# Kernel tuning notes

Hardware: AMD Instinct MI355X
Metric: run time of the kernel (lower is better)

## Reference

```python
import jax, jax.numpy as jnp
import numpy as np

N, F, E, T = 50000, 128, 800000, 8


def setup_inputs() -> dict:
    key = jax.random.key(0)
    ks = jax.random.split(key, 10)
    s = 1.0 / np.sqrt(F)
    return {
        "x": jax.random.normal(ks[0], (N, F), jnp.float32),
        "edge_index": jax.random.randint(ks[1], (2, E), 0, N, jnp.int64),
        "edge_weight": jax.random.uniform(ks[2], (E,), jnp.float32),
        "W0": jax.random.normal(ks[3], (F, F), jnp.float32) * s,
        "Wih": jax.random.normal(ks[4], (3 * F, F), jnp.float32) * s,
        "Whh": jax.random.normal(ks[5], (3 * F, F), jnp.float32) * s,
        "bih": jax.random.normal(ks[6], (3 * F,), jnp.float32) * s,
        "bhh": jax.random.normal(ks[7], (3 * F,), jnp.float32) * s,
        "Wlin": jax.random.normal(ks[8], (T, F), jnp.float32) * s,
        "blin": jax.random.normal(ks[9], (T,), jnp.float32) * s,
    }


def _evolve_weight(W0, Wih, Whh, bih, bhh):
    # One GRU step with input = hidden = W0 (rows of weight matrix as batch).
    gi = W0 @ Wih.T + bih  # [F, 3F]
    gh = W0 @ Whh.T + bhh
    ir, iz, inn = jnp.split(gi, 3, axis=1)
    hr, hz, hn = jnp.split(gh, 3, axis=1)
    r = jax.nn.sigmoid(ir + hr)
    z = jax.nn.sigmoid(iz + hz)
    n = jnp.tanh(inn + r * hn)
    return (1.0 - z) * n + z * W0  # [F, F]


def reference(x, edge_index, edge_weight, W0, Wih, Whh, bih, bhh, Wlin, blin):
    n_nodes = x.shape[0]
    W = _evolve_weight(W0, Wih, Whh, bih, bhh)
    # gcn_norm with added self-loops (fill value 1.0), symmetric normalization
    loop = jnp.arange(n_nodes, dtype=edge_index.dtype)
    row = jnp.concatenate([edge_index[0], loop])
    col = jnp.concatenate([edge_index[1], loop])
    ew = jnp.concatenate([edge_weight, jnp.ones((n_nodes,), edge_weight.dtype)])
    deg = jax.ops.segment_sum(ew, col, num_segments=n_nodes)
    dinv = jnp.where(deg > 0, jax.lax.rsqrt(jnp.where(deg > 0, deg, 1.0)), 0.0)
    norm = dinv[row] * ew * dinv[col]  # [E+N]
    xw = x @ W  # [N, F]
    h = jax.ops.segment_sum(norm[:, None] * xw[row], col, num_segments=n_nodes)
    h = jax.nn.relu(h)
    return h @ Wlin.T + blin  # [N, n_target]
```

## Files before the change

### kernel.cpp

```cpp
#include <hip/hip_runtime.h>
#include <math.h>

#define F 128
#define FIX_SCALE 16777216.0f
#define FIX_INV   (1.0f / 16777216.0f)
#define CNT_SHIFT 40
#define DEG_MASK  ((1ULL << 40) - 1)

using bf16x8 = __attribute__((ext_vector_type(8))) short;
using f32x4  = __attribute__((ext_vector_type(4))) float;

__device__ inline int read_idx(const int* ei, long long elem, int i64) {
    return i64 ? (int)((const long long*)ei)[elem] : ei[elem];
}
__device__ inline unsigned int f2bf_rn(float f) {
    unsigned int b = __float_as_uint(f);
    return (b + 0x7FFFu + ((b >> 16) & 1u)) >> 16;
}
__device__ inline float bflo(unsigned int u) { return __uint_as_float(u << 16); }
__device__ inline float bfhi(unsigned int u) { return __uint_as_float(u & 0xFFFF0000u); }

__device__ inline void acc8(float* acc, float wt, uint4 v) {
    acc[0] += wt * bflo(v.x); acc[1] += wt * bfhi(v.x);
    acc[2] += wt * bflo(v.y); acc[3] += wt * bfhi(v.y);
    acc[4] += wt * bflo(v.z); acc[5] += wt * bfhi(v.z);
    acc[6] += wt * bflo(v.w); acc[7] += wt * bfhi(v.w);
}

__global__ void k_init(unsigned long long* packed, int* flag, const int* ei, int N) {
    int i = blockIdx.x * blockDim.x + threadIdx.x;
    if (i < N) packed[i] = 0ULL;
    if (i == 0) {
        int i64 = 1;
        for (int j = 0; j < 32; ++j) if (ei[2 * j + 1] != 0) { i64 = 0; break; }
        *flag = i64;
    }
}

__global__ __launch_bounds__(256) void k_count_evolve(
        const int* __restrict__ ei, const float* __restrict__ ew,
        unsigned long long* __restrict__ packed, int* __restrict__ pos,
        const int* __restrict__ flag, int E, int cntBlocks,
        const float* __restrict__ W0, const float* __restrict__ Wih,
        const float* __restrict__ Whh, const float* __restrict__ bih,
        const float* __restrict__ bhh,
        unsigned short* __restrict__ Wth, unsigned short* __restrict__ Wtl) {
    __shared__ __align__(16) float w0row[F];
    if ((int)blockIdx.x < cntBlocks) {
        int e = blockIdx.x * 256 + threadIdx.x;
        if (e >= E) return;
        int i64 = *flag;
        int c = read_idx(ei, (long long)E + e, i64);
        unsigned long long u = (1ULL << CNT_SHIFT) |
                               (unsigned long long)(ew[e] * FIX_SCALE + 0.5f);
        unsigned long long old = atomicAdd(&packed[c], u);
        pos[e] = (int)(old >> CNT_SHIFT);
        return;
    }
    int i = blockIdx.x - cntBlocks;
    int j = threadIdx.x;
    if (j < F) w0row[j] = W0[i * F + j];
    __syncthreads();
    if (j >= F) return;
    float air = 0, aiz = 0, ain = 0, ahr = 0, ahz = 0, ahn = 0;
    const float* ir_p = Wih + (size_t)j * F;
    const float* iz_p = Wih + (size_t)(j + F) * F;
    const float* in_p = Wih + (size_t)(j + 2 * F) * F;
    const float* hr_p = Whh + (size_t)j * F;
    const float* hz_p = Whh + (size_t)(j + F) * F;
    const float* hn_p = Whh + (size_t)(j + 2 * F) * F;
    for (int k = 0; k < F; k += 4) {
        float4 w0 = *(const float4*)&w0row[k];
        float4 a;
        a = *(const float4*)&ir_p[k]; air += w0.x*a.x + w0.y*a.y + w0.z*a.z + w0.w*a.w;
        a = *(const float4*)&iz_p[k]; aiz += w0.x*a.x + w0.y*a.y + w0.z*a.z + w0.w*a.w;
        a = *(const float4*)&in_p[k]; ain += w0.x*a.x + w0.y*a.y + w0.z*a.z + w0.w*a.w;
        a = *(const float4*)&hr_p[k]; ahr += w0.x*a.x + w0.y*a.y + w0.z*a.z + w0.w*a.w;
        a = *(const float4*)&hz_p[k]; ahz += w0.x*a.x + w0.y*a.y + w0.z*a.z + w0.w*a.w;
        a = *(const float4*)&hn_p[k]; ahn += w0.x*a.x + w0.y*a.y + w0.z*a.z + w0.w*a.w;
    }
    air += bih[j];         ahr += bhh[j];
    aiz += bih[j + F];     ahz += bhh[j + F];
    ain += bih[j + 2*F];   ahn += bhh[j + 2*F];
    float r = 1.0f / (1.0f + expf(-(air + ahr)));
    float z = 1.0f / (1.0f + expf(-(aiz + ahz)));
    float n = tanhf(ain + r * ahn);
    float w = (1.0f - z) * n + z * w0row[j];
    unsigned int hb = f2bf_rn(w);
    float whi = __uint_as_float(hb << 16);
    unsigned int lb = f2bf_rn(w - whi);
    Wth[j * F + i] = (unsigned short)hb;
    Wtl[j * F + i] = (unsigned short)lb;
}

__global__ void k_bsum(const unsigned long long* __restrict__ packed,
                       int* __restrict__ bsum, int N) {
    __shared__ int s[4];
    int i = blockIdx.x * 256 + threadIdx.x;
    int v = (i < N) ? (int)(packed[i] >> CNT_SHIFT) : 0;
    #pragma unroll
    for (int o = 1; o < 64; o <<= 1) v += __shfl_xor(v, o, 64);
    if ((threadIdx.x & 63) == 0) s[threadIdx.x >> 6] = v;
    __syncthreads();
    if (threadIdx.x == 0) bsum[blockIdx.x] = s[0] + s[1] + s[2] + s[3];
}

__global__ void k_bscan(int* bsum, int nb) {
    __shared__ int sdata[1024];
    int tid = threadIdx.x;
    int run = 0;
    for (int base = 0; base < nb; base += 1024) {
        int i = base + tid;
        int v = (i < nb) ? bsum[i] : 0;
        sdata[tid] = v;
        __syncthreads();
        #pragma unroll
        for (int s = 1; s < 1024; s <<= 1) {
            int add = (tid >= s) ? sdata[tid - s] : 0;
            __syncthreads();
            sdata[tid] += add;
            __syncthreads();
        }
        if (i < nb) bsum[i] = run + sdata[tid] - v;
        run += sdata[1023];
        __syncthreads();
    }
}

__global__ void k_offs(const unsigned long long* __restrict__ packed,
                       const int* __restrict__ bsum,
                       int* __restrict__ off, float* __restrict__ dinv, int N, int E) {
    __shared__ int sdata[256];
    int t = threadIdx.x;
    int i = blockIdx.x * 256 + t;
    unsigned long long p = (i < N) ? packed[i] : 0ULL;
    int v = (int)(p >> CNT_SHIFT);
    sdata[t] = v;
    __syncthreads();
    #pragma unroll
    for (int s = 1; s < 256; s <<= 1) {
        int add = (t >= s) ? sdata[t - s] : 0;
        __syncthreads();
        sdata[t] += add;
        __syncthreads();
    }
    if (i < N) {
        off[i] = bsum[blockIdx.x] + sdata[t] - v;
        float deg = 1.0f + (float)(p & DEG_MASK) * FIX_INV;
        dinv[i] = rsqrtf(deg);
        if (i == N - 1) off[N] = E;
    }
}

__global__ __launch_bounds__(256) void k_place_cast(
        const int* __restrict__ ei, const float* __restrict__ ew,
        const int* __restrict__ off, const int* __restrict__ pos,
        int2* __restrict__ ep, const int* __restrict__ flag, int E, int placeBlocks,
        const float2* __restrict__ x2, const float* __restrict__ dinv,
        unsigned int* __restrict__ xs, int M) {
    if ((int)blockIdx.x < placeBlocks) {
        int e = blockIdx.x * 256 + threadIdx.x;
        if (e >= E) return;
        int i64 = *flag;
        int r = read_idx(ei, e, i64);
        int c = read_idx(ei, (long long)E + e, i64);
        ep[off[c] + pos[e]] = make_int2(r, __float_as_int(ew[e]));
    } else {
        int id = ((int)blockIdx.x - placeBlocks) * 256 + threadIdx.x;
        if (id >= M) return;
        float di = dinv[id >> 6];
        float2 v = x2[id];
        xs[id] = f2bf_rn(di * v.x) | (f2bf_rn(di * v.y) << 16);
    }
}

__global__ __launch_bounds__(256) void k_agg2(const uint4* __restrict__ xs4,
                                              const int* __restrict__ off,
                                              const int2* __restrict__ ep,
                                              const float* __restrict__ dinv,
                                              uint4* __restrict__ hagg4, int N) {
    int wave = threadIdx.x >> 6, lane = threadIdx.x & 63;
    int c = blockIdx.x * 4 + wave;
    if (c >= N) return;
    int g = lane >> 4, sl = lane & 15;
    int start = off[c], end = off[c + 1];
    float di = dinv[c];
    float a0[8] = {0,0,0,0,0,0,0,0}, a1[8] = {0,0,0,0,0,0,0,0};
    if (g == 0) {
        uint4 v = xs4[(size_t)c * 16 + sl];
        a0[0] = bflo(v.x); a0[1] = bfhi(v.x);
        a0[2] = bflo(v.y); a0[3] = bfhi(v.y);
        a0[4] = bflo(v.z); a0[5] = bfhi(v.z);
        a0[6] = bflo(v.w); a0[7] = bfhi(v.w);
    }
    int last = end - 1;
    for (int k = start; k < end; k += 16) {
        int iA = k + g, iB = k + g + 4, iC = k + g + 8, iD = k + g + 12;
        int2 eA = ep[min(iA, last)];
        int2 eB = ep[min(iB, last)];
        int2 eC = ep[min(iC, last)];
        int2 eD = ep[min(iD, last)];
        uint4 vA = xs4[(size_t)eA.x * 16 + sl];
        uint4 vB = xs4[(size_t)eB.x * 16 + sl];
        uint4 vC = xs4[(size_t)eC.x * 16 + sl];
        uint4 vD = xs4[(size_t)eD.x * 16 + sl];
        float wA = (iA <= last) ? __int_as_float(eA.y) : 0.f;
        float wB = (iB <= last) ? __int_as_float(eB.y) : 0.f;
        float wC = (iC <= last) ? __int_as_float(eC.y) : 0.f;
        float wD = (iD <= last) ? __int_as_float(eD.y) : 0.f;
        acc8(a0, wA, vA);
        acc8(a1, wB, vB);
        acc8(a0, wC, vC);
        acc8(a1, wD, vD);
    }
    #pragma unroll
    for (int f = 0; f < 8; ++f) {
        float v = a0[f] + a1[f];
        v += __shfl_xor(v, 16, 64);
        v += __shfl_xor(v, 32, 64);
        a0[f] = v;
    }
    if (lane < 16) {
        uint4 o;
        o.x = f2bf_rn(di * a0[0]) | (f2bf_rn(di * a0[1]) << 16);
        o.y = f2bf_rn(di * a0[2]) | (f2bf_rn(di * a0[3]) << 16);
        o.z = f2bf_rn(di * a0[4]) | (f2bf_rn(di * a0[5]) << 16);
        o.w = f2bf_rn(di * a0[6]) | (f2bf_rn(di * a0[7]) << 16);
        hagg4[(size_t)c * 16 + lane] = o;
    }
}

__global__ __launch_bounds__(256) void k_gemm(const uint4* __restrict__ hagg4,
                                              const unsigned short* __restrict__ Wth,
                                              const unsigned short* __restrict__ Wtl,
                                              const float* __restrict__ Wlin,
                                              const float* __restrict__ blin,
                                              float* __restrict__ out, int N) {
    __shared__ __align__(16) unsigned int At[64 * 68];
    __shared__ __align__(16) float WlinL[8 * F];
    int t = threadIdx.x;
    int row0 = blockIdx.x * 64;
    #pragma unroll
    for (int it = 0; it < 4; ++it) {
        int idx = it * 256 + t;
        int rr = idx >> 4, c4 = idx & 15;
        uint4 v = make_uint4(0u, 0u, 0u, 0u);
        if (row0 + rr < N) v = hagg4[(size_t)(row0 + rr) * 16 + c4];
        *(uint4*)&At[rr * 68 + c4 * 4] = v;
    }
    *(float4*)&WlinL[t * 4] = *(const float4*)&Wlin[t * 4];
    __syncthreads();

    int wave = t >> 6, lane = t & 63;
    int sl = lane & 15, q = lane >> 4;
    const unsigned short* Ash = (const unsigned short*)At;
    int mrow = wave * 16 + sl;

    f32x4 acc[8];
    #pragma unroll
    for (int nt = 0; nt < 8; ++nt) acc[nt] = (f32x4){0.f, 0.f, 0.f, 0.f};
    #pragma unroll
    for (int ko = 0; ko < 4; ++ko) {
        bf16x8 a = *(const bf16x8*)&Ash[mrow * 136 + ko * 32 + q * 8];
        #pragma unroll
        for (int nt = 0; nt < 8; ++nt) {
            int boff = (nt * 16 + sl) * F + ko * 32 + q * 8;
            bf16x8 bh = *(const bf16x8*)&Wth[boff];
            bf16x8 bl = *(const bf16x8*)&Wtl[boff];
            acc[nt] = __builtin_amdgcn_mfma_f32_16x16x32_bf16(a, bh, acc[nt], 0, 0, 0);
            acc[nt] = __builtin_amdgcn_mfma_f32_16x16x32_bf16(a, bl, acc[nt], 0, 0, 0);
        }
    }
    #pragma unroll
    for (int nt = 0; nt < 8; ++nt)
        #pragma unroll
        for (int r = 0; r < 4; ++r) acc[nt][r] = fmaxf(acc[nt][r], 0.f);

    float p[8][4];
    #pragma unroll
    for (int tt = 0; tt < 8; ++tt) {
        float wl[8];
        #pragma unroll
        for (int nt = 0; nt < 8; ++nt) wl[nt] = WlinL[tt * F + nt * 16 + sl];
        #pragma unroll
        for (int r = 0; r < 4; ++r) {
            float s = 0.f;
            #pragma unroll
            for (int nt = 0; nt < 8; ++nt) s += acc[nt][r] * wl[nt];
            p[tt][r] = s;
        }
    }
    #pragma unroll
    for (int tt = 0; tt < 8; ++tt)
        #pragma unroll
        for (int r = 0; r < 4; ++r) {
            float v = p[tt][r];
            v += __shfl_xor(v, 1, 64); v += __shfl_xor(v, 2, 64);
            v += __shfl_xor(v, 4, 64); v += __shfl_xor(v, 8, 64);
            p[tt][r] = v;
        }
    if (sl == 0) {
        #pragma unroll
        for (int r = 0; r < 4; ++r) {
            int row = row0 + wave * 16 + q * 4 + r;
            if (row < N) {
                #pragma unroll
                for (int tt = 0; tt < 8; ++tt)
                    out[(size_t)row * 8 + tt] = p[tt][r] + blin[tt];
            }
        }
    }
}

extern "C" void kernel_launch(void* const* d_in, const int* in_sizes, int n_in,
                              void* d_out, int out_size, void* d_ws, size_t ws_size,
                              hipStream_t stream) {
    const float* x    = (const float*)d_in[0];
    const int*   ei   = (const int*)d_in[1];
    const float* ew   = (const float*)d_in[2];
    const float* W0   = (const float*)d_in[3];
    const float* Wih  = (const float*)d_in[4];
    const float* Whh  = (const float*)d_in[5];
    const float* bih  = (const float*)d_in[6];
    const float* bhh  = (const float*)d_in[7];
    const float* Wlin = (const float*)d_in[8];
    const float* blin = (const float*)d_in[9];
    int N = in_sizes[0] / F;
    int E = in_sizes[1] / 2;
    float* outp = (float*)d_out;

    int nblk = (N + 255) / 256;
    int cntBlocks = (E + 255) / 256;
    int M = N * 64;

    char* wsb = (char*)d_ws;
    size_t cur = 0;
    auto alloc = [&](size_t sz) -> void* {
        void* p = wsb + cur;
        cur = (cur + sz + 255) & ~(size_t)255;
        return p;
    };
    unsigned long long* packed = (unsigned long long*)alloc((size_t)N * 8);
    float* dinv = (float*)alloc((size_t)N * 4);
    int*   off  = (int*)  alloc((size_t)(N + 1) * 4);
    int*   bsum = (int*)  alloc((size_t)nblk * 4);
    int*   flag = (int*)  alloc(256);
    int*   pos  = (int*)  alloc((size_t)E * 4);
    int2*  ep   = (int2*) alloc((size_t)E * 8);
    unsigned short* Wth = (unsigned short*)alloc((size_t)F * F * 2);
    unsigned short* Wtl = (unsigned short*)alloc((size_t)F * F * 2);
    unsigned int* xs    = (unsigned int*)alloc((size_t)N * 64 * 4);
    unsigned int* hagg  = (unsigned int*)alloc((size_t)N * 64 * 4);
    (void)ws_size; (void)n_in; (void)out_size;

    hipLaunchKernelGGL(k_init, dim3(nblk), dim3(256), 0, stream, packed, flag, ei, N);
    hipLaunchKernelGGL(k_count_evolve, dim3(cntBlocks + F), dim3(256), 0, stream,
                       ei, ew, packed, pos, flag, E, cntBlocks,
                       W0, Wih, Whh, bih, bhh, Wth, Wtl);
    hipLaunchKernelGGL(k_bsum,  dim3(nblk), dim3(256),  0, stream, packed, bsum, N);
    hipLaunchKernelGGL(k_bscan, dim3(1),    dim3(1024), 0, stream, bsum, nblk);
    hipLaunchKernelGGL(k_offs,  dim3(nblk), dim3(256),  0, stream, packed, bsum, off, dinv, N, E);
    hipLaunchKernelGGL(k_place_cast, dim3(cntBlocks + (M + 255) / 256), dim3(256), 0, stream,
                       ei, ew, off, pos, ep, flag, E, cntBlocks,
                       (const float2*)x, dinv, xs, M);
    hipLaunchKernelGGL(k_agg2, dim3((N + 3) / 4), dim3(256), 0, stream,
                       (const uint4*)xs, off, ep, dinv, (uint4*)hagg, N);
    hipLaunchKernelGGL(k_gemm, dim3((N + 63) / 64), dim3(256), 0, stream,
                       (const uint4*)hagg, Wth, Wtl, Wlin, blin, outp, N);
}
```

Baseline: 249.9 us.

## Privatize degree atomics across eight copies and spread GRU evolve over waves

The per-destination count/degree atomics now go to one of eight replicated counters, chosen by block index, which cuts contention on the same address. Per-copy bases are computed in k_offs and stored so placement can still produce a deterministic CSR slot. The GRU weight evolution moves from 128 blocks of 128 threads to 256 blocks in which each wave handles 16 output pairs, with the K loop split four ways and reduced by shuffles. The cost is eight times the counter memory plus extra reads in bsum/offs and an extra copyBase lookup during placement.

```diff
diff --git a/kernel.cpp b/kernel.cpp
--- a/kernel.cpp
+++ b/kernel.cpp
@@ -6,6 +6,7 @@
 #define FIX_INV   (1.0f / 16777216.0f)
 #define CNT_SHIFT 40
 #define DEG_MASK  ((1ULL << 40) - 1)
+#define EVB 256
 
 using bf16x8 = __attribute__((ext_vector_type(8))) short;
 using f32x4  = __attribute__((ext_vector_type(4))) float;
@@ -27,9 +28,9 @@
     acc[6] += wt * bflo(v.w); acc[7] += wt * bfhi(v.w);
 }
 
-__global__ void k_init(unsigned long long* packed, int* flag, const int* ei, int N) {
+__global__ void k_init(unsigned long long* packed8, int* flag, const int* ei, int M8) {
     int i = blockIdx.x * blockDim.x + threadIdx.x;
-    if (i < N) packed[i] = 0ULL;
+    if (i < M8) packed8[i] = 0ULL;
     if (i == 0) {
         int i64 = 1;
         for (int j = 0; j < 32; ++j) if (ei[2 * j + 1] != 0) { i64 = 0; break; }
@@ -39,65 +40,84 @@
 
 __global__ __launch_bounds__(256) void k_count_evolve(
         const int* __restrict__ ei, const float* __restrict__ ew,
-        unsigned long long* __restrict__ packed, int* __restrict__ pos,
-        const int* __restrict__ flag, int E, int cntBlocks,
+        unsigned long long* __restrict__ packed8, int* __restrict__ pos,
+        const int* __restrict__ flag, int E, int N,
         const float* __restrict__ W0, const float* __restrict__ Wih,
         const float* __restrict__ Whh, const float* __restrict__ bih,
         const float* __restrict__ bhh,
         unsigned short* __restrict__ Wth, unsigned short* __restrict__ Wtl) {
-    __shared__ __align__(16) float w0row[F];
-    if ((int)blockIdx.x < cntBlocks) {
-        int e = blockIdx.x * 256 + threadIdx.x;
+    int wave = threadIdx.x >> 6, lane = threadIdx.x & 63;
+    if ((int)blockIdx.x >= EVB) {
+        int e = ((int)blockIdx.x - EVB) * 256 + threadIdx.x;
         if (e >= E) return;
         int i64 = *flag;
         int c = read_idx(ei, (long long)E + e, i64);
+        int copy = blockIdx.x & 7;
         unsigned long long u = (1ULL << CNT_SHIFT) |
                                (unsigned long long)(ew[e] * FIX_SCALE + 0.5f);
-        unsigned long long old = atomicAdd(&packed[c], u);
-        pos[e] = (int)(old >> CNT_SHIFT);
+        unsigned long long old = atomicAdd(&packed8[(size_t)copy * N + c], u);
+        pos[e] = (int)(((unsigned int)(old >> CNT_SHIFT)) | ((unsigned int)copy << 24));
         return;
     }
-    int i = blockIdx.x - cntBlocks;
-    int j = threadIdx.x;
-    if (j < F) w0row[j] = W0[i * F + j];
-    __syncthreads();
-    if (j >= F) return;
+    int gw = (int)blockIdx.x * 4 + wave;
+    int pairBase = gw * 16;
+    int i = pairBase >> 7;
+    int jb = pairBase & 127;
+    int lp = lane & 15, sl = lane >> 4;
+    int j = jb + lp;
+    const float* w0p = W0 + (size_t)i * F;
+    const float* pir = Wih + (size_t)j * F;
+    const float* piz = Wih + (size_t)(j + F) * F;
+    const float* pin = Wih + (size_t)(j + 2 * F) * F;
+    const float* phr = Whh + (size_t)j * F;
+    const float* phz = Whh + (size_t)(j + F) * F;
+    const float* phn = Whh + (size_t)(j + 2 * F) * F;
     float air = 0, aiz = 0, ain = 0, ahr = 0, ahz = 0, ahn = 0;
-    const float* ir_p = Wih + (size_t)j * F;
-    const float* iz_p = Wih + (size_t)(j + F) * F;
-    const float* in_p = Wih + (size_t)(j + 2 * F) * F;
-    const float* hr_p = Whh + (size_t)j * F;
-    const float* hz_p = Whh + (size_t)(j + F) * F;
-    const float* hn_p = Whh + (size_t)(j + 2 * F) * F;
-    for (int k = 0; k < F; k += 4) {
-        float4 w0 = *(const float4*)&w0row[k];
+    int k0 = sl * 32;
+    #pragma unroll
+    for (int kk = 0; kk < 32; kk += 4) {
+        int k = k0 + kk;
+        float4 w0 = *(const float4*)&w0p[k];
         float4 a;
-        a = *(const float4*)&ir_p[k]; air += w0.x*a.x + w0.y*a.y + w0.z*a.z + w0.w*a.w;
-        a = *(const float4*)&iz_p[k]; aiz += w0.x*a.x + w0.y*a.y + w0.z*a.z + w0.w*a.w;
-        a = *(const float4*)&in_p[k]; ain += w0.x*a.x + w0.y*a.y + w0.z*a.z + w0.w*a.w;
-        a = *(const float4*)&hr_p[k]; ahr += w0.x*a.x + w0.y*a.y + w0.z*a.z + w0.w*a.w;
-        a = *(const float4*)&hz_p[k]; ahz += w0.x*a.x + w0.y*a.y + w0.z*a.z + w0.w*a.w;
-        a = *(const float4*)&hn_p[k]; ahn += w0.x*a.x + w0.y*a.y + w0.z*a.z + w0.w*a.w;
-    }
-    air += bih[j];         ahr += bhh[j];
-    aiz += bih[j + F];     ahz += bhh[j + F];
-    ain += bih[j + 2*F];   ahn += bhh[j + 2*F];
-    float r = 1.0f / (1.0f + expf(-(air + ahr)));
-    float z = 1.0f / (1.0f + expf(-(aiz + ahz)));
-    float n = tanhf(ain + r * ahn);
-    float w = (1.0f - z) * n + z * w0row[j];
-    unsigned int hb = f2bf_rn(w);
-    float whi = __uint_as_float(hb << 16);
-    unsigned int lb = f2bf_rn(w - whi);
-    Wth[j * F + i] = (unsigned short)hb;
-    Wtl[j * F + i] = (unsigned short)lb;
-}
-
-__global__ void k_bsum(const unsigned long long* __restrict__ packed,
+        a = *(const float4*)&pir[k]; air += w0.x*a.x + w0.y*a.y + w0.z*a.z + w0.w*a.w;
+        a = *(const float4*)&piz[k]; aiz += w0.x*a.x + w0.y*a.y + w0.z*a.z + w0.w*a.w;
+        a = *(const float4*)&pin[k]; ain += w0.x*a.x + w0.y*a.y + w0.z*a.z + w0.w*a.w;
+        a = *(const float4*)&phr[k]; ahr += w0.x*a.x + w0.y*a.y + w0.z*a.z + w0.w*a.w;
+        a = *(const float4*)&phz[k]; ahz += w0.x*a.x + w0.y*a.y + w0.z*a.z + w0.w*a.w;
+        a = *(const float4*)&phn[k]; ahn += w0.x*a.x + w0.y*a.y + w0.z*a.z + w0.w*a.w;
+    }
+    air += __shfl_xor(air, 16, 64); air += __shfl_xor(air, 32, 64);
+    aiz += __shfl_xor(aiz, 16, 64); aiz += __shfl_xor(aiz, 32, 64);
+    ain += __shfl_xor(ain, 16, 64); ain += __shfl_xor(ain, 32, 64);
+    ahr += __shfl_xor(ahr, 16, 64); ahr += __shfl_xor(ahr, 32, 64);
+    ahz += __shfl_xor(ahz, 16, 64); ahz += __shfl_xor(ahz, 32, 64);
+    ahn += __shfl_xor(ahn, 16, 64); ahn += __shfl_xor(ahn, 32, 64);
+    if (sl == 0) {
+        air += bih[j];          ahr += bhh[j];
+        aiz += bih[j + F];      ahz += bhh[j + F];
+        ain += bih[j + 2 * F];  ahn += bhh[j + 2 * F];
+        float r = 1.0f / (1.0f + expf(-(air + ahr)));
+        float z = 1.0f / (1.0f + expf(-(aiz + ahz)));
+        float n = tanhf(ain + r * ahn);
+        float w = (1.0f - z) * n + z * w0p[j];
+        unsigned int hb = f2bf_rn(w);
+        float whi = __uint_as_float(hb << 16);
+        unsigned int lb = f2bf_rn(w - whi);
+        Wth[j * F + i] = (unsigned short)hb;
+        Wtl[j * F + i] = (unsigned short)lb;
+    }
+}
+
+__global__ void k_bsum(const unsigned long long* __restrict__ packed8,
                        int* __restrict__ bsum, int N) {
     __shared__ int s[4];
     int i = blockIdx.x * 256 + threadIdx.x;
-    int v = (i < N) ? (int)(packed[i] >> CNT_SHIFT) : 0;
+    int v = 0;
+    if (i < N) {
+        #pragma unroll
+        for (int k = 0; k < 8; ++k)
+            v += (int)(packed8[(size_t)k * N + i] >> CNT_SHIFT);
+    }
     #pragma unroll
     for (int o = 1; o < 64; o <<= 1) v += __shfl_xor(v, o, 64);
     if ((threadIdx.x & 63) == 0) s[threadIdx.x >> 6] = v;
@@ -127,14 +147,29 @@
     }
 }
 
-__global__ void k_offs(const unsigned long long* __restrict__ packed,
+__global__ void k_offs(const unsigned long long* __restrict__ packed8,
                        const int* __restrict__ bsum,
-                       int* __restrict__ off, float* __restrict__ dinv, int N, int E) {
+                       int* __restrict__ off, int* __restrict__ copyBase,
+                       float* __restrict__ dinv, int N, int E) {
     __shared__ int sdata[256];
     int t = threadIdx.x;
     int i = blockIdx.x * 256 + t;
-    unsigned long long p = (i < N) ? packed[i] : 0ULL;
-    int v = (int)(p >> CNT_SHIFT);
+    int v = 0;
+    unsigned long long dsum = 0;
+    int cb[8];
+    if (i < N) {
+        int run = 0;
+        #pragma unroll
+        for (int k = 0; k < 8; ++k) {
+            unsigned long long p = packed8[(size_t)k * N + i];
+            cb[k] = run;
+            run += (int)(p >> CNT_SHIFT);
+            dsum += (p & DEG_MASK);
+        }
+        v = run;
+        #pragma unroll
+        for (int k = 0; k < 8; ++k) copyBase[(size_t)i * 8 + k] = cb[k];
+    }
     sdata[t] = v;
     __syncthreads();
     #pragma unroll
@@ -146,7 +181,7 @@
     }
     if (i < N) {
         off[i] = bsum[blockIdx.x] + sdata[t] - v;
-        float deg = 1.0f + (float)(p & DEG_MASK) * FIX_INV;
+        float deg = 1.0f + (float)dsum * FIX_INV;
         dinv[i] = rsqrtf(deg);
         if (i == N - 1) off[N] = E;
     }
@@ -154,7 +189,8 @@
 
 __global__ __launch_bounds__(256) void k_place_cast(
         const int* __restrict__ ei, const float* __restrict__ ew,
-        const int* __restrict__ off, const int* __restrict__ pos,
+        const int* __restrict__ off, const int* __restrict__ copyBase,
+        const int* __restrict__ pos,
         int2* __restrict__ ep, const int* __restrict__ flag, int E, int placeBlocks,
         const float2* __restrict__ x2, const float* __restrict__ dinv,
         unsigned int* __restrict__ xs, int M) {
@@ -164,7 +200,9 @@
         int i64 = *flag;
         int r = read_idx(ei, e, i64);
         int c = read_idx(ei, (long long)E + e, i64);
-        ep[off[c] + pos[e]] = make_int2(r, __float_as_int(ew[e]));
+        int pe = pos[e];
+        int slot = off[c] + copyBase[(size_t)c * 8 + (pe >> 24)] + (pe & 0xFFFFFF);
+        ep[slot] = make_int2(r, __float_as_int(ew[e]));
     } else {
         int id = ((int)blockIdx.x - placeBlocks) * 256 + threadIdx.x;
         if (id >= M) return;
@@ -332,6 +370,7 @@
     int nblk = (N + 255) / 256;
     int cntBlocks = (E + 255) / 256;
     int M = N * 64;
+    int M8 = N * 8;
 
     char* wsb = (char*)d_ws;
     size_t cur = 0;
@@ -340,12 +379,13 @@
         cur = (cur + sz + 255) & ~(size_t)255;
         return p;
     };
-    unsigned long long* packed = (unsigned long long*)alloc((size_t)N * 8);
+    unsigned long long* packed8 = (unsigned long long*)alloc((size_t)M8 * 8);
     float* dinv = (float*)alloc((size_t)N * 4);
     int*   off  = (int*)  alloc((size_t)(N + 1) * 4);
     int*   bsum = (int*)  alloc((size_t)nblk * 4);
     int*   flag = (int*)  alloc(256);
     int*   pos  = (int*)  alloc((size_t)E * 4);
+    int*   copyBase = (int*)alloc((size_t)N * 8 * 4);
     int2*  ep   = (int2*) alloc((size_t)E * 8);
     unsigned short* Wth = (unsigned short*)alloc((size_t)F * F * 2);
     unsigned short* Wtl = (unsigned short*)alloc((size_t)F * F * 2);
@@ -353,15 +393,15 @@
     unsigned int* hagg  = (unsigned int*)alloc((size_t)N * 64 * 4);
     (void)ws_size; (void)n_in; (void)out_size;
 
-    hipLaunchKernelGGL(k_init, dim3(nblk), dim3(256), 0, stream, packed, flag, ei, N);
-    hipLaunchKernelGGL(k_count_evolve, dim3(cntBlocks + F), dim3(256), 0, stream,
-                       ei, ew, packed, pos, flag, E, cntBlocks,
+    hipLaunchKernelGGL(k_init, dim3((M8 + 255) / 256), dim3(256), 0, stream, packed8, flag, ei, M8);
+    hipLaunchKernelGGL(k_count_evolve, dim3(EVB + cntBlocks), dim3(256), 0, stream,
+                       ei, ew, packed8, pos, flag, E, N,
                        W0, Wih, Whh, bih, bhh, Wth, Wtl);
-    hipLaunchKernelGGL(k_bsum,  dim3(nblk), dim3(256),  0, stream, packed, bsum, N);
+    hipLaunchKernelGGL(k_bsum,  dim3(nblk), dim3(256),  0, stream, packed8, bsum, N);
     hipLaunchKernelGGL(k_bscan, dim3(1),    dim3(1024), 0, stream, bsum, nblk);
-    hipLaunchKernelGGL(k_offs,  dim3(nblk), dim3(256),  0, stream, packed, bsum, off, dinv, N, E);
+    hipLaunchKernelGGL(k_offs,  dim3(nblk), dim3(256),  0, stream, packed8, bsum, off, copyBase, dinv, N, E);
     hipLaunchKernelGGL(k_place_cast, dim3(cntBlocks + (M + 255) / 256), dim3(256), 0, stream,
-                       ei, ew, off, pos, ep, flag, E, cntBlocks,
+                       ei, ew, off, copyBase, pos, ep, flag, E, cntBlocks,
                        (const float2*)x, dinv, xs, M);
     hipLaunchKernelGGL(k_agg2, dim3((N + 3) / 4), dim3(256), 0, stream,
                        (const uint4*)xs, off, ep, dinv, (uint4*)hagg, N);
```

Measured after the change: 219.6 us. 12.1% less time.
